# Optimization experiments

Measured on AMD Instinct MI355X. Metric: run time of the kernel, lower is better.

Reference implementation:

```python
import jax, jax.numpy as jnp
import numpy as np

TOKENS, HIDDEN, N_EXPERTS = 16384, 2048, 64
JITTER_EPS = 0.01
Z_LOSS_COEFF = 0.001


def setup_inputs() -> dict:
    key = jax.random.key(0)
    k1, k2 = jax.random.split(key)
    x = jax.random.normal(k1, (TOKENS, HIDDEN), dtype=jnp.float32)
    w = jax.random.normal(k2, (N_EXPERTS, HIDDEN), dtype=jnp.float32) * 0.02  # router weight [E,H]
    return {"x": x, "w": w}


def _route_pass(scores_sel, scores, jitter_eps):
    # scores_sel: logits possibly with -inf at already-selected expert (top-2 pass)
    # scores:     original logits (used for abs/clamp factor, as in torch code)
    mx = jnp.max(scores_sel, axis=-1, keepdims=True)                      # [N,1]
    factor = jnp.maximum(jnp.abs(scores), mx)                             # scores.abs().clamp(min=mx)
    mask = jax.lax.stop_gradient((mx - scores) / factor > 2.0 * jitter_eps)
    masked_logits = jnp.where(mask, -jnp.inf, scores_sel)
    # eval path (training=False): selected_experts = argmax of (masked-for-selection) scores
    sel = jnp.argmax(scores_sel, axis=-1)[..., None]                      # [N,1] int
    gates = jax.nn.softmax(masked_logits, axis=-1)
    # mask_for_one: selected == argmax(gates) holds deterministically in eval -> 1.0
    mult = jnp.take_along_axis(gates, sel, axis=-1)                       # [N,1]
    return mult, sel


def reference(x, w):
    logits = x @ w.T                                                      # [N,E]
    # z-loss (identity on logits in forward; scalar returned for completeness)
    z_loss = Z_LOSS_COEFF * jnp.mean(jnp.square(jax.nn.logsumexp(logits, axis=-1)))
    original_gates = jax.nn.softmax(logits, axis=-1)
    # top-1 pass
    m1, s1 = _route_pass(logits, logits, JITTER_EPS)
    # top-2 pass: mask out the first selection
    e_idx = jnp.arange(logits.shape[-1])[None, :]
    scores2 = jnp.where(e_idx == s1, -jnp.inf, logits)
    m2, s2 = _route_pass(scores2, logits, JITTER_EPS)
    multiplier = jnp.concatenate([m1, m2], axis=-1)                       # [N,2]
    selected_experts = jnp.concatenate([s1, s2], axis=-1)                 # [N,2]
    return multiplier, original_gates, selected_experts, z_loss
```

## Files before the change

kernel.cpp:

```cpp
#include <hip/hip_runtime.h>
#include <math.h>

#define TOKENS 16384
#define HIDDEN 2048
#define NEXP   64
#define MT     16
#define NBLK   (TOKENS / MT)
#define BK     256
#define NCH    (HIDDEN / BK)
#define CB     16384

#define GATES_OFF (TOKENS * 2)
#define SEL_OFF   (GATES_OFF + TOKENS * NEXP)
#define Z_OFF     (SEL_OFF + TOKENS * 2)

#define WIMG_BYTES (NEXP * HIDDEN * 2 * 2)

typedef __attribute__((ext_vector_type(8))) _Float16 f16x8;
typedef __attribute__((ext_vector_type(4))) float    f32x4;

__device__ __forceinline__ float wave_sum64(float v) {
    #pragma unroll
    for (int s = 1; s < 64; s <<= 1) v += __shfl_xor(v, s, 64);
    return v;
}

__device__ __forceinline__ void dma16(const void* g, void* l) {
    __builtin_amdgcn_global_load_lds(
        (const __attribute__((address_space(1))) unsigned int*)g,
        (__attribute__((address_space(3))) unsigned int*)l, 16, 0, 0);
}

__global__ __launch_bounds__(256) void wconvert(
    const float* __restrict__ w, uint4* __restrict__ wimg)
{
    const int s = blockIdx.x * 256 + threadIdx.x;
    const int c    = s >> 10;
    const int r    = s & 1023;
    const int l    = r & 63;
    const int nt   = (r >> 6) & 1;
    const int kh   = (r >> 7) & 1;
    const int term = (r >> 8) & 1;
    const int eh   = (r >> 9) & 1;
    const int e = eh * 32 + nt * 16 + (l & 15);
    const int k = c * 64 + kh * 32 + (l >> 4) * 8;

    const float* src = w + (size_t)e * HIDDEN + k;
    union { _Float16 f[8]; uint4 u; } o;
    #pragma unroll
    for (int j = 0; j < 8; ++j) {
        const float v = src[j];
        const _Float16 h = (_Float16)v;
        o.f[j] = (term == 0) ? h : (_Float16)((v - (float)h) * 4096.f);
    }
    wimg[s] = o.u;
}

__device__ __forceinline__ void cvt_split(const float4 a, const float4 b,
                                          f16x8& hi, f16x8& lo) {
    union { _Float16 f[8]; f16x8 v; } H, L;
    #pragma unroll
    for (int j = 0; j < 4; ++j) {
        const float s0 = (&a.x)[j];
        const float s1 = (&b.x)[j];
        const _Float16 h0 = (_Float16)s0;
        const _Float16 h1 = (_Float16)s1;
        H.f[j]     = h0;
        H.f[j + 4] = h1;
        L.f[j]     = (_Float16)((s0 - (float)h0) * 4096.f);
        L.f[j + 4] = (_Float16)((s1 - (float)h1) * 4096.f);
    }
    hi = H.v; lo = L.v;
}

__global__ __launch_bounds__(64) void router_main(
    const float* __restrict__ x, const uint4* __restrict__ wimg,
    float* __restrict__ out, float* __restrict__ zpartial)
{
    __shared__ __align__(16) unsigned char smem[2 * CB];

    const int lane = threadIdx.x & 63;
    const int t0   = blockIdx.x * MT;
    const int rowr = lane & 15;
    const int kg   = lane >> 4;

    const float* xq = x + (size_t)(t0 + rowr) * HIDDEN + kg * 4;

    f32x4 acc0[4], acc1[4];
    #pragma unroll
    for (int g = 0; g < 4; ++g) { acc0[g] = (f32x4)0.f; acc1[g] = (f32x4)0.f; }

    #pragma unroll
    for (int j = 0; j < 16; ++j)
        dma16(xq + j * 16, smem + j * 1024);

    for (int c = 0; c < NCH; ++c) {
        asm volatile("s_waitcnt vmcnt(0)" ::: "memory");
        __builtin_amdgcn_sched_barrier(0);

        if (c + 1 < NCH) {
            const float* sg = xq + (c + 1) * BK;
            unsigned char* dg = smem + ((c + 1) & 1) * CB;
            #pragma unroll
            for (int j = 0; j < 16; ++j)
                dma16(sg + j * 16, dg + j * 1024);
        }

        const unsigned char* ab = smem + (c & 1) * CB + kg * 512 + rowr * 16;
        const uint4* wc0 = wimg + (size_t)c * 4096 + lane;
        #pragma unroll
        for (int s = 0; s < 8; ++s) {
            const uint4* p = wc0 + (s >> 1) * 1024 + (s & 1) * 128;
            f16x8 bh[4], bl[4];
            bh[0] = *(const f16x8*)(p);
            bh[1] = *(const f16x8*)(p + 64);
            bh[2] = *(const f16x8*)(p + 512);
            bh[3] = *(const f16x8*)(p + 576);
            bl[0] = *(const f16x8*)(p + 256);
            bl[1] = *(const f16x8*)(p + 320);
            bl[2] = *(const f16x8*)(p + 768);
            bl[3] = *(const f16x8*)(p + 832);

            const float4 va = *(const float4*)(ab + s * 2048);
            const float4 vb = *(const float4*)(ab + s * 2048 + 256);
            f16x8 Ah, Al;
            cvt_split(va, vb, Ah, Al);
            #pragma unroll
            for (int g = 0; g < 4; ++g) {
                acc0[g] = __builtin_amdgcn_mfma_f32_16x16x32_f16(Ah, bh[g], acc0[g], 0, 0, 0);
                acc1[g] = __builtin_amdgcn_mfma_f32_16x16x32_f16(Ah, bl[g], acc1[g], 0, 0, 0);
                acc1[g] = __builtin_amdgcn_mfma_f32_16x16x32_f16(Al, bh[g], acc1[g], 0, 0, 0);
            }
        }
    }

    float zsum = 0.f;
    #pragma unroll
    for (int r = 0; r < 4; ++r) {
        const int t = kg * 4 + r;
        float v[4]; int e[4];
        #pragma unroll
        for (int g = 0; g < 4; ++g) {
            v[g] = acc0[g][r] + acc1[g][r] * (1.f / 4096.f);
            e[g] = g * 16 + rowr;
        }

        float bv = v[0]; int bi = e[0];
        #pragma unroll
        for (int g = 1; g < 4; ++g)
            if (v[g] > bv) { bv = v[g]; bi = e[g]; }
        #pragma unroll
        for (int st = 1; st < 16; st <<= 1) {
            const float ov = __shfl_xor(bv, st, 64);
            const int   oi = __shfl_xor(bi, st, 64);
            if (ov > bv || (ov == bv && oi < bi)) { bv = ov; bi = oi; }
        }
        const float max1 = bv; const int s1 = bi;

        float e1[4], se = 0.f, sm1 = 0.f;
        #pragma unroll
        for (int g = 0; g < 4; ++g) {
            e1[g] = expf(v[g] - max1);
            se += e1[g];
            const bool m1 = (max1 - v[g]) > 0.02f * fmaxf(fabsf(v[g]), max1);
            sm1 += m1 ? 0.f : e1[g];
        }
        #pragma unroll
        for (int st = 1; st < 16; st <<= 1) {
            se  += __shfl_xor(se, st, 64);
            sm1 += __shfl_xor(sm1, st, 64);
        }

        #pragma unroll
        for (int g = 0; g < 4; ++g)
            out[GATES_OFF + (size_t)(t0 + t) * NEXP + e[g]] = e1[g] / se;

        const float lse = max1 + logf(se);
        if (rowr == 0) zsum += lse * lse;

        float bv2 = (e[0] == s1) ? -INFINITY : v[0]; int bi2 = e[0];
        #pragma unroll
        for (int g = 1; g < 4; ++g) {
            const float cv = (e[g] == s1) ? -INFINITY : v[g];
            if (cv > bv2) { bv2 = cv; bi2 = e[g]; }
        }
        #pragma unroll
        for (int st = 1; st < 16; st <<= 1) {
            const float ov = __shfl_xor(bv2, st, 64);
            const int   oi = __shfl_xor(bi2, st, 64);
            if (ov > bv2 || (ov == bv2 && oi < bi2)) { bv2 = ov; bi2 = oi; }
        }
        const float max2 = bv2; const int s2 = bi2;

        float sm2 = 0.f;
        #pragma unroll
        for (int g = 0; g < 4; ++g) {
            const bool m2 = (max2 - v[g]) > 0.02f * fmaxf(fabsf(v[g]), max2);
            sm2 += (m2 || e[g] == s1) ? 0.f : expf(v[g] - max2);
        }
        #pragma unroll
        for (int st = 1; st < 16; st <<= 1)
            sm2 += __shfl_xor(sm2, st, 64);

        if (rowr == 0) {
            const size_t trow = (size_t)(t0 + t) * 2;
            out[trow + 0] = 1.f / sm1;
            out[trow + 1] = 1.f / sm2;
            out[SEL_OFF + trow + 0] = (float)s1;
            out[SEL_OFF + trow + 1] = (float)s2;
        }
    }

    const float zt = wave_sum64(zsum);
    if (lane == 0) zpartial[blockIdx.x] = zt;
}

__global__ __launch_bounds__(256) void zfinal(
    const float* __restrict__ zpartial, float* __restrict__ out)
{
    const int tid = threadIdx.x;
    float v = zpartial[tid] + zpartial[tid + 256]
            + zpartial[tid + 512] + zpartial[tid + 768];
    v = wave_sum64(v);
    __shared__ float red[4];
    if ((tid & 63) == 0) red[tid >> 6] = v;
    __syncthreads();
    if (tid == 0) {
        const float tot = red[0] + red[1] + red[2] + red[3];
        out[Z_OFF] = 0.001f * (tot / (float)TOKENS);
    }
}

extern "C" void kernel_launch(void* const* d_in, const int* in_sizes, int n_in,
                              void* d_out, int out_size, void* d_ws, size_t ws_size,
                              hipStream_t stream) {
    const float* x = (const float*)d_in[0];
    const float* w = (const float*)d_in[1];
    float* out = (float*)d_out;

    uint4* wimg     = (uint4*)d_ws;
    float* zpartial = (float*)((char*)d_ws + WIMG_BYTES);

    wconvert<<<128, 256, 0, stream>>>(w, wimg);
    router_main<<<NBLK, 64, 0, stream>>>(x, wimg, out, zpartial);
    zfinal<<<1, 256, 0, stream>>>(zpartial, out);
}
```

Before: 236.2 us.

## Replace split-fp16 MFMA router GEMM with fp32 FMA split-K kernel

Drops the weight pre-conversion kernel and the three-MFMA fp16 hi/lo emulation. Each block of four waves now handles 32 tokens, with every wave computing a quarter of K using plain fp32 FMAs directly from global memory. Partial logits are reduced through shared memory before the routing epilogue, and gate stores become float4 writes. This removes the conversion pass and the split-precision overhead. The cost is running on scalar FP32 ALUs instead of matrix cores, with heavy uncoalesced global loads and no LDS staging of x.

```diff
diff --git a/kernel.cpp b/kernel.cpp
--- a/kernel.cpp
+++ b/kernel.cpp
@@ -4,20 +4,12 @@
 #define TOKENS 16384
 #define HIDDEN 2048
 #define NEXP   64
-#define MT     16
+#define MT     32
 #define NBLK   (TOKENS / MT)
-#define BK     256
-#define NCH    (HIDDEN / BK)
-#define CB     16384
 
 #define GATES_OFF (TOKENS * 2)
 #define SEL_OFF   (GATES_OFF + TOKENS * NEXP)
 #define Z_OFF     (SEL_OFF + TOKENS * 2)
-
-#define WIMG_BYTES (NEXP * HIDDEN * 2 * 2)
-
-typedef __attribute__((ext_vector_type(8))) _Float16 f16x8;
-typedef __attribute__((ext_vector_type(4))) float    f32x4;
 
 __device__ __forceinline__ float wave_sum64(float v) {
     #pragma unroll
@@ -25,130 +17,74 @@
     return v;
 }
 
-__device__ __forceinline__ void dma16(const void* g, void* l) {
-    __builtin_amdgcn_global_load_lds(
-        (const __attribute__((address_space(1))) unsigned int*)g,
-        (__attribute__((address_space(3))) unsigned int*)l, 16, 0, 0);
-}
-
-__global__ __launch_bounds__(256) void wconvert(
-    const float* __restrict__ w, uint4* __restrict__ wimg)
-{
-    const int s = blockIdx.x * 256 + threadIdx.x;
-    const int c    = s >> 10;
-    const int r    = s & 1023;
-    const int l    = r & 63;
-    const int nt   = (r >> 6) & 1;
-    const int kh   = (r >> 7) & 1;
-    const int term = (r >> 8) & 1;
-    const int eh   = (r >> 9) & 1;
-    const int e = eh * 32 + nt * 16 + (l & 15);
-    const int k = c * 64 + kh * 32 + (l >> 4) * 8;
-
-    const float* src = w + (size_t)e * HIDDEN + k;
-    union { _Float16 f[8]; uint4 u; } o;
-    #pragma unroll
-    for (int j = 0; j < 8; ++j) {
-        const float v = src[j];
-        const _Float16 h = (_Float16)v;
-        o.f[j] = (term == 0) ? h : (_Float16)((v - (float)h) * 4096.f);
-    }
-    wimg[s] = o.u;
-}
-
-__device__ __forceinline__ void cvt_split(const float4 a, const float4 b,
-                                          f16x8& hi, f16x8& lo) {
-    union { _Float16 f[8]; f16x8 v; } H, L;
-    #pragma unroll
-    for (int j = 0; j < 4; ++j) {
-        const float s0 = (&a.x)[j];
-        const float s1 = (&b.x)[j];
-        const _Float16 h0 = (_Float16)s0;
-        const _Float16 h1 = (_Float16)s1;
-        H.f[j]     = h0;
-        H.f[j + 4] = h1;
-        L.f[j]     = (_Float16)((s0 - (float)h0) * 4096.f);
-        L.f[j + 4] = (_Float16)((s1 - (float)h1) * 4096.f);
-    }
-    hi = H.v; lo = L.v;
-}
-
-__global__ __launch_bounds__(64) void router_main(
-    const float* __restrict__ x, const uint4* __restrict__ wimg,
+__global__ __launch_bounds__(256, 2) void router_fma(
+    const float* __restrict__ x, const float* __restrict__ w,
     float* __restrict__ out, float* __restrict__ zpartial)
 {
-    __shared__ __align__(16) unsigned char smem[2 * CB];
+    __shared__ __align__(16) float lg[4][MT][66];
+    __shared__ float zred[4];
 
-    const int lane = threadIdx.x & 63;
+    const int tid  = threadIdx.x;
+    const int wv   = __builtin_amdgcn_readfirstlane(tid >> 6);
+    const int lane = tid & 63;
+    const int eg   = lane & 15;
+    const int tl   = lane >> 4;
     const int t0   = blockIdx.x * MT;
-    const int rowr = lane & 15;
-    const int kg   = lane >> 4;
 
-    const float* xq = x + (size_t)(t0 + rowr) * HIDDEN + kg * 4;
+    const float* xp = x + (size_t)(t0 + tl * 8) * HIDDEN + wv * 512;
+    const float* wp = w + (size_t)(eg * 4) * HIDDEN + wv * 512;
 
-    f32x4 acc0[4], acc1[4];
+    float acc[8][4];
     #pragma unroll
-    for (int g = 0; g < 4; ++g) { acc0[g] = (f32x4)0.f; acc1[g] = (f32x4)0.f; }
+    for (int j = 0; j < 8; ++j)
+        #pragma unroll
+        for (int e = 0; e < 4; ++e) acc[j][e] = 0.f;
+
+    #pragma unroll 2
+    for (int kk = 0; kk < 512; kk += 4) {
+        float4 xv[8], wv4[4];
+        #pragma unroll
+        for (int j = 0; j < 8; ++j)
+            xv[j] = *(const float4*)(xp + (size_t)j * HIDDEN + kk);
+        #pragma unroll
+        for (int e = 0; e < 4; ++e)
+            wv4[e] = *(const float4*)(wp + (size_t)e * HIDDEN + kk);
+
+        #pragma unroll
+        for (int j = 0; j < 8; ++j)
+            #pragma unroll
+            for (int e = 0; e < 4; ++e) {
+                acc[j][e] = fmaf(xv[j].x, wv4[e].x, acc[j][e]);
+                acc[j][e] = fmaf(xv[j].y, wv4[e].y, acc[j][e]);
+                acc[j][e] = fmaf(xv[j].z, wv4[e].z, acc[j][e]);
+                acc[j][e] = fmaf(xv[j].w, wv4[e].w, acc[j][e]);
+            }
+    }
 
     #pragma unroll
-    for (int j = 0; j < 16; ++j)
-        dma16(xq + j * 16, smem + j * 1024);
-
-    for (int c = 0; c < NCH; ++c) {
-        asm volatile("s_waitcnt vmcnt(0)" ::: "memory");
-        __builtin_amdgcn_sched_barrier(0);
-
-        if (c + 1 < NCH) {
-            const float* sg = xq + (c + 1) * BK;
-            unsigned char* dg = smem + ((c + 1) & 1) * CB;
-            #pragma unroll
-            for (int j = 0; j < 16; ++j)
-                dma16(sg + j * 16, dg + j * 1024);
-        }
-
-        const unsigned char* ab = smem + (c & 1) * CB + kg * 512 + rowr * 16;
-        const uint4* wc0 = wimg + (size_t)c * 4096 + lane;
+    for (int j = 0; j < 8; ++j)
         #pragma unroll
-        for (int s = 0; s < 8; ++s) {
-            const uint4* p = wc0 + (s >> 1) * 1024 + (s & 1) * 128;
-            f16x8 bh[4], bl[4];
-            bh[0] = *(const f16x8*)(p);
-            bh[1] = *(const f16x8*)(p + 64);
-            bh[2] = *(const f16x8*)(p + 512);
-            bh[3] = *(const f16x8*)(p + 576);
-            bl[0] = *(const f16x8*)(p + 256);
-            bl[1] = *(const f16x8*)(p + 320);
-            bl[2] = *(const f16x8*)(p + 768);
-            bl[3] = *(const f16x8*)(p + 832);
-
-            const float4 va = *(const float4*)(ab + s * 2048);
-            const float4 vb = *(const float4*)(ab + s * 2048 + 256);
-            f16x8 Ah, Al;
-            cvt_split(va, vb, Ah, Al);
-            #pragma unroll
-            for (int g = 0; g < 4; ++g) {
-                acc0[g] = __builtin_amdgcn_mfma_f32_16x16x32_f16(Ah, bh[g], acc0[g], 0, 0, 0);
-                acc1[g] = __builtin_amdgcn_mfma_f32_16x16x32_f16(Ah, bl[g], acc1[g], 0, 0, 0);
-                acc1[g] = __builtin_amdgcn_mfma_f32_16x16x32_f16(Al, bh[g], acc1[g], 0, 0, 0);
-            }
-        }
-    }
+        for (int e = 0; e < 4; ++e)
+            lg[wv][tl * 8 + j][eg * 4 + e] = acc[j][e];
+    __syncthreads();
 
     float zsum = 0.f;
+    const int tt = lane >> 4;
     #pragma unroll
-    for (int r = 0; r < 4; ++r) {
-        const int t = kg * 4 + r;
+    for (int r2 = 0; r2 < 2; ++r2) {
+        const int tloc = wv * 8 + r2 * 4 + tt;
         float v[4]; int e[4];
         #pragma unroll
-        for (int g = 0; g < 4; ++g) {
-            v[g] = acc0[g][r] + acc1[g][r] * (1.f / 4096.f);
-            e[g] = g * 16 + rowr;
+        for (int j = 0; j < 4; ++j) {
+            v[j] = lg[0][tloc][eg * 4 + j] + lg[1][tloc][eg * 4 + j]
+                 + lg[2][tloc][eg * 4 + j] + lg[3][tloc][eg * 4 + j];
+            e[j] = eg * 4 + j;
         }
 
         float bv = v[0]; int bi = e[0];
         #pragma unroll
-        for (int g = 1; g < 4; ++g)
-            if (v[g] > bv) { bv = v[g]; bi = e[g]; }
+        for (int j = 1; j < 4; ++j)
+            if (v[j] > bv) { bv = v[j]; bi = e[j]; }
         #pragma unroll
         for (int st = 1; st < 16; st <<= 1) {
             const float ov = __shfl_xor(bv, st, 64);
@@ -159,11 +95,11 @@
 
         float e1[4], se = 0.f, sm1 = 0.f;
         #pragma unroll
-        for (int g = 0; g < 4; ++g) {
-            e1[g] = expf(v[g] - max1);
-            se += e1[g];
-            const bool m1 = (max1 - v[g]) > 0.02f * fmaxf(fabsf(v[g]), max1);
-            sm1 += m1 ? 0.f : e1[g];
+        for (int j = 0; j < 4; ++j) {
+            e1[j] = expf(v[j] - max1);
+            se += e1[j];
+            const bool m1 = (max1 - v[j]) > 0.02f * fmaxf(fabsf(v[j]), max1);
+            sm1 += m1 ? 0.f : e1[j];
         }
         #pragma unroll
         for (int st = 1; st < 16; st <<= 1) {
@@ -171,18 +107,21 @@
             sm1 += __shfl_xor(sm1, st, 64);
         }
 
-        #pragma unroll
-        for (int g = 0; g < 4; ++g)
-            out[GATES_OFF + (size_t)(t0 + t) * NEXP + e[g]] = e1[g] / se;
+        {
+            float4 gv;
+            gv.x = e1[0] / se; gv.y = e1[1] / se;
+            gv.z = e1[2] / se; gv.w = e1[3] / se;
+            *(float4*)(out + GATES_OFF + (size_t)(t0 + tloc) * NEXP + eg * 4) = gv;
+        }
 
         const float lse = max1 + logf(se);
-        if (rowr == 0) zsum += lse * lse;
+        if (eg == 0) zsum += lse * lse;
 
         float bv2 = (e[0] == s1) ? -INFINITY : v[0]; int bi2 = e[0];
         #pragma unroll
-        for (int g = 1; g < 4; ++g) {
-            const float cv = (e[g] == s1) ? -INFINITY : v[g];
-            if (cv > bv2) { bv2 = cv; bi2 = e[g]; }
+        for (int j = 1; j < 4; ++j) {
+            const float cv = (e[j] == s1) ? -INFINITY : v[j];
+            if (cv > bv2) { bv2 = cv; bi2 = e[j]; }
         }
         #pragma unroll
         for (int st = 1; st < 16; st <<= 1) {
@@ -194,16 +133,16 @@
 
         float sm2 = 0.f;
         #pragma unroll
-        for (int g = 0; g < 4; ++g) {
-            const bool m2 = (max2 - v[g]) > 0.02f * fmaxf(fabsf(v[g]), max2);
-            sm2 += (m2 || e[g] == s1) ? 0.f : expf(v[g] - max2);
+        for (int j = 0; j < 4; ++j) {
+            const bool m2 = (max2 - v[j]) > 0.02f * fmaxf(fabsf(v[j]), max2);
+            sm2 += (m2 || e[j] == s1) ? 0.f : expf(v[j] - max2);
         }
         #pragma unroll
         for (int st = 1; st < 16; st <<= 1)
             sm2 += __shfl_xor(sm2, st, 64);
 
-        if (rowr == 0) {
-            const size_t trow = (size_t)(t0 + t) * 2;
+        if (eg == 0) {
+            const size_t trow = (size_t)(t0 + tloc) * 2;
             out[trow + 0] = 1.f / sm1;
             out[trow + 1] = 1.f / sm2;
             out[SEL_OFF + trow + 0] = (float)s1;
@@ -212,15 +151,17 @@
     }
 
     const float zt = wave_sum64(zsum);
-    if (lane == 0) zpartial[blockIdx.x] = zt;
+    if (lane == 0) zred[wv] = zt;
+    __syncthreads();
+    if (tid == 0)
+        zpartial[blockIdx.x] = zred[0] + zred[1] + zred[2] + zred[3];
 }
 
 __global__ __launch_bounds__(256) void zfinal(
     const float* __restrict__ zpartial, float* __restrict__ out)
 {
     const int tid = threadIdx.x;
-    float v = zpartial[tid] + zpartial[tid + 256]
-            + zpartial[tid + 512] + zpartial[tid + 768];
+    float v = zpartial[tid] + zpartial[tid + 256];
     v = wave_sum64(v);
     __shared__ float red[4];
     if ((tid & 63) == 0) red[tid >> 6] = v;
@@ -238,10 +179,8 @@
     const float* w = (const float*)d_in[1];
     float* out = (float*)d_out;
 
-    uint4* wimg     = (uint4*)d_ws;
-    float* zpartial = (float*)((char*)d_ws + WIMG_BYTES);
+    float* zpartial = (float*)d_ws;
 
-    wconvert<<<128, 256, 0, stream>>>(w, wimg);
-    router_main<<<NBLK, 64, 0, stream>>>(x, wimg, out, zpartial);
+    router_fma<<<NBLK, 256, 0, stream>>>(x, w, out, zpartial);
     zfinal<<<1, 256, 0, stream>>>(zpartial, out);
 }
```

Measured after the change: 335.5 us. 1.42x slower.
